# Optimization experiments

Measured on AMD Instinct MI355X. Metric: run time of the kernel, lower is better.

Reference implementation:

```python
import jax, jax.numpy as jnp
import numpy as np

D_MODEL, D_STATE, D_CONV, EXPAND = 1024, 16, 4, 2
D_INNER = EXPAND * D_MODEL
DT_RANK = (D_MODEL + 15) // 16  # 64
B_SZ, SEQ = 2, 1024


def _mamba_dir(x, inW, convW, convB, xpW, dtW, dtB, Alog, Dp, outW):
    """Standard Mamba block forward. x: [B, L, d_model]."""
    Bsz, L, _ = x.shape
    d_inner, d_state = Alog.shape
    dt_rank = xpW.shape[0] - 2 * d_state
    xz = jnp.einsum('bld,ed->ble', x, inW)            # [B, L, 2*d_inner]
    xi, z = jnp.split(xz, 2, axis=-1)
    # depthwise causal conv along L
    xc = jnp.swapaxes(xi, 1, 2)                       # [B, d_inner, L]
    xc = jax.lax.conv_general_dilated(
        xc, convW, window_strides=(1,),
        padding=[(convW.shape[-1] - 1, 0)],
        feature_group_count=d_inner)
    xc = xc + convB[None, :, None]
    u = jax.nn.silu(jnp.swapaxes(xc, 1, 2))           # [B, L, d_inner]
    x_dbl = jnp.einsum('bld,ed->ble', u, xpW)         # [B, L, dt_rank+2N]
    dt, Bm, Cm = jnp.split(x_dbl, [dt_rank, dt_rank + d_state], axis=-1)
    delta = jax.nn.softplus(jnp.einsum('blr,dr->bld', dt, dtW) + dtB)  # [B,L,d_inner]
    A = -jnp.exp(Alog)                                # [d_inner, d_state]

    def step(h, ins):
        d_t, B_t, C_t, u_t = ins                      # [B,D],[B,N],[B,N],[B,D]
        dA = jnp.exp(d_t[:, :, None] * A)             # [B, D, N]
        h = h * dA + (d_t * u_t)[:, :, None] * B_t[:, None, :]
        y_t = jnp.einsum('bdn,bn->bd', h, C_t)
        return h, y_t

    h0 = jnp.zeros((Bsz, d_inner, d_state), x.dtype)
    xs = (jnp.swapaxes(delta, 0, 1), jnp.swapaxes(Bm, 0, 1),
          jnp.swapaxes(Cm, 0, 1), jnp.swapaxes(u, 0, 1))
    _, ys = jax.lax.scan(step, h0, xs)
    y = jnp.swapaxes(ys, 0, 1)                        # [B, L, d_inner]
    y = y + u * Dp
    y = y * jax.nn.silu(z)
    return jnp.einsum('bld,od->blo', y, outW)         # [B, L, d_model]


def _make_params(key, suffix):
    ks = jax.random.split(key, 10)
    s = 0.02
    p = {
        'inW' + suffix: jax.random.normal(ks[0], (2 * D_INNER, D_MODEL), jnp.float32) * s,
        'convW' + suffix: jax.random.normal(ks[1], (D_INNER, 1, D_CONV), jnp.float32) * s,
        'convB' + suffix: jnp.zeros((D_INNER,), jnp.float32),
        'xpW' + suffix: jax.random.normal(ks[2], (DT_RANK + 2 * D_STATE, D_INNER), jnp.float32) * s,
        'dtW' + suffix: jax.random.normal(ks[3], (D_INNER, DT_RANK), jnp.float32) * s,
        'dtB' + suffix: jax.random.normal(ks[4], (D_INNER,), jnp.float32) * 0.1 - 4.0,
        'Alog' + suffix: jnp.log(1.0 + jax.random.uniform(ks[5], (D_INNER, D_STATE), jnp.float32) * 15.0),
        'Dp' + suffix: jnp.ones((D_INNER,), jnp.float32),
        'outW' + suffix: jax.random.normal(ks[6], (D_MODEL, D_INNER), jnp.float32) * s,
    }
    return p


def setup_inputs() -> dict:
    key = jax.random.key(0)
    kx, kf, kb = jax.random.split(key, 3)
    inp = {'x': jax.random.normal(kx, (B_SZ, SEQ, D_MODEL), jnp.float32)}
    inp.update(_make_params(kf, '_f'))
    inp.update(_make_params(kb, '_b'))
    return inp


def reference(x, inW_f, convW_f, convB_f, xpW_f, dtW_f, dtB_f, Alog_f, Dp_f, outW_f,
              inW_b, convW_b, convB_b, xpW_b, dtW_b, dtB_b, Alog_b, Dp_b, outW_b):
    y_fwd = _mamba_dir(x, inW_f, convW_f, convB_f, xpW_f, dtW_f, dtB_f, Alog_f, Dp_f, outW_f)
    xb = jnp.flip(x, axis=1)
    y_bwd = jnp.flip(_mamba_dir(xb, inW_b, convW_b, convB_b, xpW_b, dtW_b, dtB_b, Alog_b, Dp_b, outW_b), axis=1)
    return 0.5 * (y_fwd + y_bwd)
```

## Files before the change

### kernel.cpp

```cpp
#include <hip/hip_runtime.h>
#include <math.h>

#define B_SZ 2
#define SEQ  1024
#define DM   1024
#define DI   2048
#define NST  16
#define RNK  64
#define XPD  96
#define M_TOT (B_SZ*SEQ)
#define NC   32
#define LC   (SEQ/NC)
#define NCH  65536

typedef unsigned short ushort_t;
typedef __attribute__((ext_vector_type(8))) short short8;
typedef __attribute__((ext_vector_type(4))) float f32x4;

#if __has_builtin(__builtin_amdgcn_exp2f)
#define EXP2F __builtin_amdgcn_exp2f
#else
#define EXP2F exp2f
#endif
#define LOG2E 1.44269504f

__device__ __forceinline__ ushort_t f2bf(float f) {
    unsigned u = __float_as_uint(f);
    u += 0x7fff + ((u >> 16) & 1);
    return (ushort_t)(u >> 16);
}
__device__ __forceinline__ float bf2f(ushort_t v) {
    return __uint_as_float(((unsigned)v) << 16);
}

__global__ __launch_bounds__(256)
void convert_all(const float* __restrict__ x,
                 const float* __restrict__ inWf, const float* __restrict__ inWb,
                 const float* __restrict__ outWf, const float* __restrict__ outWb,
                 const float* __restrict__ xpWf, const float* __restrict__ xpWb,
                 ushort_t* __restrict__ xbf, ushort_t* __restrict__ inWcat,
                 ushort_t* __restrict__ outWcat, ushort_t* __restrict__ xpWcat)
{
    int bid = blockIdx.x;
    const float* src; ushort_t* dst; int rel; int strided = 0;
    if (bid < 2048)       { rel = bid;         src = x;     dst = xbf; }
    else if (bid < 6144)  { rel = bid - 2048;  src = inWf;  dst = inWcat; }
    else if (bid < 10240) { rel = bid - 6144;  src = inWb;  dst = inWcat + (size_t)2 * DI * DM; }
    else if (bid < 12288) { rel = bid - 10240; src = outWf; dst = outWcat;      strided = 1; }
    else if (bid < 14336) { rel = bid - 12288; src = outWb; dst = outWcat + DI; strided = 1; }
    else if (bid < 14528) { rel = bid - 14336; src = xpWf;  dst = xpWcat; }
    else                  { rel = bid - 14528; src = xpWb;  dst = xpWcat + (size_t)XPD * DI; }
    int i = rel * 256 + threadIdx.x;
    float4 v = ((const float4*)src)[i];
    ushort4 o;
    o.x = f2bf(v.x); o.y = f2bf(v.y); o.z = f2bf(v.z); o.w = f2bf(v.w);
    if (!strided) {
        ((ushort4*)dst)[i] = o;
    } else {
        int row = i >> 9;
        int c4  = (i - (row << 9)) << 2;
        *(ushort4*)(dst + (size_t)row * (2 * DI) + c4) = o;
    }
}

__device__ __forceinline__ void load_lds16(const ushort_t* g, ushort_t* l) {
    __builtin_amdgcn_global_load_lds(
        (const __attribute__((address_space(1))) void*)g,
        (__attribute__((address_space(3))) void*)l, 16, 0, 0);
}

__device__ __forceinline__ void stageHalf(const ushort_t* g, int grow0, int K, int kt,
                                          ushort_t* lds, int w8, int l8, int gch)
{
    const ushort_t* p = g + (size_t)(grow0 + w8 + l8) * K + (size_t)kt * 64 + (gch << 3);
    load_lds16(p,                  lds + w8 * 64);
    load_lds16(p + (size_t)64 * K, lds + (64 + w8) * 64);
}

__device__ __forceinline__ void rdA4(const ushort_t* buf, int rbase, int sw0, int sw1,
                                     short8 (&a)[4][2])
{
#pragma unroll
    for (int i = 0; i < 4; i++) {
        const ushort_t* p = buf + (size_t)(rbase + i * 16) * 64;
        a[i][0] = *(const short8*)(p + sw0);
        a[i][1] = *(const short8*)(p + sw1);
    }
}
__device__ __forceinline__ void rdB2(const ushort_t* buf, int rbase, int sw0, int sw1,
                                     short8 (&bb)[2][2])
{
#pragma unroll
    for (int j = 0; j < 2; j++) {
        const ushort_t* p = buf + (size_t)(rbase + j * 16) * 64;
        bb[j][0] = *(const short8*)(p + sw0);
        bb[j][1] = *(const short8*)(p + sw1);
    }
}
__device__ __forceinline__ void mm16(const short8 (&a)[4][2], const short8 (&bb)[2][2],
                                     f32x4 (&acc)[4][2])
{
#pragma unroll
    for (int i = 0; i < 4; i++)
#pragma unroll
        for (int j = 0; j < 2; j++) {
            acc[i][j] = __builtin_amdgcn_mfma_f32_16x16x32_bf16(a[i][0], bb[j][0], acc[i][j], 0, 0, 0);
            acc[i][j] = __builtin_amdgcn_mfma_f32_16x16x32_bf16(a[i][1], bb[j][1], acc[i][j], 0, 0, 0);
        }
}

#define BAR()        __builtin_amdgcn_s_barrier()
#define SCHEDB()     __builtin_amdgcn_sched_barrier(0)
#define PRIO1()      __builtin_amdgcn_s_setprio(1)
#define PRIO0()      __builtin_amdgcn_s_setprio(0)
#define WAIT_LGKM0() asm volatile("s_waitcnt lgkmcnt(0)" ::: "memory")
#define WAIT_VM6()   asm volatile("s_waitcnt vmcnt(6)"  ::: "memory")
#define WAIT_VM0()   asm volatile("s_waitcnt vmcnt(0)"  ::: "memory")

__global__ __launch_bounds__(512, 2)
void gemm256_bf16(const ushort_t* __restrict__ A, const ushort_t* __restrict__ W,
                  ushort_t* __restrict__ D, int K, int ldD)
{
    __shared__ __align__(16) ushort_t As[2][256 * 64];
    __shared__ __align__(16) ushort_t Bs[2][256 * 64];

    const int t_   = threadIdx.x;
    const int lane = t_ & 63;
    const int wave = t_ >> 6;
    const int wrq  = wave >> 2;
    const int wcq  = wave & 3;
    const int lm   = lane & 15;
    const int w8   = wave << 3;
    const int l8   = lane >> 3;
    const int gch  = (lane & 7) ^ l8;
    const int sw0  = (((lane >> 4)    ) ^ (lane & 7)) << 3;
    const int sw1  = (((lane >> 4) + 4) ^ (lane & 7)) << 3;

    const int m0 = blockIdx.y * 256;
    const int n0 = blockIdx.x * 256;
    const int NT = K >> 6;

    const int rA0 = wrq * 64 + lm, rA1 = 128 + rA0;
    const int rB0 = wcq * 32 + lm, rB1 = 128 + rB0;

    f32x4 acc[2][2][4][2] = {};
    short8 a[4][2], b0[2][2], b1[2][2];

    stageHalf(A, m0,       K, 0, &As[0][0],        w8, l8, gch);
    stageHalf(A, m0 + 128, K, 0, &As[0][128 * 64], w8, l8, gch);
    stageHalf(W, n0,       K, 0, &Bs[0][0],        w8, l8, gch);
    stageHalf(W, n0 + 128, K, 0, &Bs[0][128 * 64], w8, l8, gch);
    if (NT > 1) {
        stageHalf(A, m0,       K, 1, &As[1][0],        w8, l8, gch);
        stageHalf(W, n0,       K, 1, &Bs[1][0],        w8, l8, gch);
        stageHalf(W, n0 + 128, K, 1, &Bs[1][128 * 64], w8, l8, gch);
        WAIT_VM6();
    } else {
        WAIT_VM0();
    }
    BAR();

    for (int t = 0; t < NT; ++t) {
        const int b = t & 1;
        const ushort_t* Ab = &As[b][0];
        const ushort_t* Bb = &Bs[b][0];
        ushort_t* Abw = &As[b][0];
        ushort_t* Bbw = &Bs[b][0];
        ushort_t* Aow = &As[b ^ 1][0];

        rdA4(Ab, rA0, sw0, sw1, a);
        rdB2(Bb, rB0, sw0, sw1, b0);
        if (t + 1 < NT) stageHalf(A, m0 + 128, K, t + 1, Aow + 128 * 64, w8, l8, gch);
        SCHEDB(); BAR(); WAIT_LGKM0(); SCHEDB();
        PRIO1(); mm16(a, b0, acc[0][0]); PRIO0();
        SCHEDB(); BAR();

        rdB2(Bb, rB1, sw0, sw1, b1);
        if (t + 2 < NT) stageHalf(A, m0, K, t + 2, Abw, w8, l8, gch);
        SCHEDB(); BAR(); WAIT_LGKM0(); SCHEDB();
        PRIO1(); mm16(a, b1, acc[0][1]); PRIO0();
        SCHEDB(); BAR();

        rdA4(Ab, rA1, sw0, sw1, a);
        if (t + 2 < NT) stageHalf(W, n0, K, t + 2, Bbw, w8, l8, gch);
        SCHEDB(); BAR(); WAIT_LGKM0(); SCHEDB();
        PRIO1(); mm16(a, b1, acc[1][1]); PRIO0();
        SCHEDB(); BAR();

        if (t + 2 < NT) stageHalf(W, n0 + 128, K, t + 2, Bbw + 128 * 64, w8, l8, gch);
        SCHEDB(); BAR();
        PRIO1(); mm16(a, b0, acc[1][0]); PRIO0();
        SCHEDB();
        if (t < NT - 2) { WAIT_VM6(); } else { WAIT_VM0(); }
        BAR();
    }

#pragma unroll
    for (int ih = 0; ih < 2; ih++)
#pragma unroll
        for (int i = 0; i < 4; i++)
#pragma unroll
            for (int r = 0; r < 4; r++) {
                int m = m0 + ih * 128 + wrq * 64 + i * 16 + ((lane >> 4) << 2) + r;
#pragma unroll
                for (int jh = 0; jh < 2; jh++)
#pragma unroll
                    for (int j = 0; j < 2; j++) {
                        int n = n0 + jh * 128 + wcq * 32 + j * 16 + lm;
                        D[(size_t)m * ldD + n] = f2bf(acc[ih][jh][i][j][r]);
                    }
            }
}

template<bool OUT_BF16>
__global__ __launch_bounds__(256)
void gemm_gll(const ushort_t* __restrict__ A, const ushort_t* __restrict__ W,
              void* __restrict__ D, int M, int N, int K, int kLen, int ldD)
{
    __shared__ __align__(16) ushort_t As[128 * 64];
    __shared__ __align__(16) ushort_t Ws[128 * 64];
    const int t    = threadIdx.x;
    const int lane = t & 63;
    const int wave = t >> 6;
    const int wr   = (wave >> 1) * 64;
    const int wc   = (wave & 1) * 64;

    const int m0 = blockIdx.y * 128;
    const int n0 = blockIdx.x * 128;
    const int kStart = blockIdx.z * kLen;

    const int srow   = lane >> 3;
    const int gchunk = (lane & 7) ^ srow;

    f32x4 acc[4][4] = {};

    for (int k0 = kStart; k0 < kStart + kLen; k0 += 64) {
#pragma unroll
        for (int it = 0; it < 4; it++) {
            const int rb = wave * 32 + it * 8;
            load_lds16(A + (size_t)(m0 + rb + srow) * K + k0 + gchunk * 8,
                       As + rb * 64);
            load_lds16(W + (size_t)(n0 + rb + srow) * K + k0 + gchunk * 8,
                       Ws + rb * 64);
        }
        __syncthreads();
#pragma unroll
        for (int kk = 0; kk < 2; kk++) {
            const int kc = kk * 4 + (lane >> 4);
            short8 af[4], bf[4];
#pragma unroll
            for (int i = 0; i < 4; i++) {
                int r = wr + i * 16 + (lane & 15);
                af[i] = *(const short8*)(As + r * 64 + ((kc ^ (r & 7)) << 3));
            }
#pragma unroll
            for (int j = 0; j < 4; j++) {
                int r = wc + j * 16 + (lane & 15);
                bf[j] = *(const short8*)(Ws + r * 64 + ((kc ^ (r & 7)) << 3));
            }
#pragma unroll
            for (int i = 0; i < 4; i++)
#pragma unroll
                for (int j = 0; j < 4; j++)
                    acc[i][j] = __builtin_amdgcn_mfma_f32_16x16x32_bf16(
                        af[i], bf[j], acc[i][j], 0, 0, 0);
        }
        __syncthreads();
    }

    if (OUT_BF16) {
        ushort_t* Dp = (ushort_t*)D;
#pragma unroll
        for (int i = 0; i < 4; i++)
#pragma unroll
            for (int r = 0; r < 4; r++) {
                int m = m0 + wr + i * 16 + ((lane >> 4) << 2) + r;
#pragma unroll
                for (int j = 0; j < 4; j++) {
                    int n = n0 + wc + j * 16 + (lane & 15);
                    Dp[(size_t)m * ldD + n] = f2bf(acc[i][j][r]);
                }
            }
    } else {
        float* Dp = (float*)D + (size_t)blockIdx.z * M * ldD;
#pragma unroll
        for (int i = 0; i < 4; i++)
#pragma unroll
            for (int r = 0; r < 4; r++) {
                int m = m0 + wr + i * 16 + ((lane >> 4) << 2) + r;
#pragma unroll
                for (int j = 0; j < 4; j++) {
                    int n = n0 + wc + j * 16 + (lane & 15);
                    Dp[(size_t)m * ldD + n] = acc[i][j][r];
                }
            }
    }
}

__global__ __launch_bounds__(256)
void reduce4(const float* __restrict__ P, float* __restrict__ out)
{
    int i = blockIdx.x * 256 + threadIdx.x;
    const size_t S = (size_t)M_TOT * DM / 4;
    float4 a = ((const float4*)P)[i];
    float4 b = ((const float4*)P)[i + S];
    float4 c = ((const float4*)P)[i + 2 * S];
    float4 d = ((const float4*)P)[i + 3 * S];
    float4 o;
    o.x = 0.5f * (a.x + b.x + c.x + d.x);
    o.y = 0.5f * (a.y + b.y + c.y + d.y);
    o.z = 0.5f * (a.z + b.z + c.z + d.z);
    o.w = 0.5f * (a.w + b.w + c.w + d.w);
    ((float4*)out)[i] = o;
}

#define LDSP 72

__global__ __launch_bounds__(256)
void gemm2_splitk2(const ushort_t* __restrict__ ubf, const ushort_t* __restrict__ xpWcat,
                   float* __restrict__ P)
{
    const int dir = blockIdx.z >> 3;
    const int kz  = blockIdx.z & 7;
    const ushort_t* A = ubf + (size_t)dir * M_TOT * DI;
    const ushort_t* W = xpWcat + (size_t)dir * XPD * DI;
    const int K = DI, N = XPD;

    __shared__ __align__(16) ushort_t As[64 * LDSP];
    __shared__ __align__(16) ushort_t Ws[64 * LDSP];
    const int t    = threadIdx.x;
    const int lane = t & 63;
    const int wave = t >> 6;
    const int wr   = (wave >> 1) * 32;
    const int wc   = (wave & 1) * 32;

    f32x4 acc[2][2] = {};

    const int m0 = blockIdx.y * 64;
    const int n0 = blockIdx.x * 64;
    const int kStart = kz * (DI / 8);
    const int srow = t >> 3;
    const int scol = (t & 7) << 3;

    for (int k0 = kStart; k0 < kStart + DI / 8; k0 += 64) {
        {
            int r = srow;
            short8 v = *(const short8*)(A + (size_t)(m0 + r) * K + k0 + scol);
            *(short8*)(&As[r * LDSP + scol]) = v;
            int r2 = 32 + srow;
            short8 v2 = *(const short8*)(A + (size_t)(m0 + r2) * K + k0 + scol);
            *(short8*)(&As[r2 * LDSP + scol]) = v2;
            int wn = n0 + r;
            short8 wv = {};
            if (wn < N) wv = *(const short8*)(W + (size_t)wn * K + k0 + scol);
            *(short8*)(&Ws[r * LDSP + scol]) = wv;
            int wn2 = n0 + r2;
            short8 wv2 = {};
            if (wn2 < N) wv2 = *(const short8*)(W + (size_t)wn2 * K + k0 + scol);
            *(short8*)(&Ws[r2 * LDSP + scol]) = wv2;
        }
        __syncthreads();
#pragma unroll
        for (int kk = 0; kk < 2; kk++) {
            const int kcol = kk * 32 + ((lane >> 4) << 3);
            short8 af[2], bfr[2];
#pragma unroll
            for (int i = 0; i < 2; i++)
                af[i] = *(const short8*)(&As[(wr + i * 16 + (lane & 15)) * LDSP + kcol]);
#pragma unroll
            for (int j = 0; j < 2; j++)
                bfr[j] = *(const short8*)(&Ws[(wc + j * 16 + (lane & 15)) * LDSP + kcol]);
#pragma unroll
            for (int i = 0; i < 2; i++)
#pragma unroll
                for (int j = 0; j < 2; j++)
                    acc[i][j] = __builtin_amdgcn_mfma_f32_16x16x32_bf16(
                        af[i], bfr[j], acc[i][j], 0, 0, 0);
        }
        __syncthreads();
    }

    float* Pz = P + ((size_t)dir * 8 + kz) * M_TOT * XPD;
#pragma unroll
    for (int i = 0; i < 2; i++)
#pragma unroll
        for (int r = 0; r < 4; r++) {
            int m = m0 + wr + i * 16 + ((lane >> 4) << 2) + r;
#pragma unroll
            for (int j = 0; j < 2; j++) {
                int n = n0 + wc + j * 16 + (lane & 15);
                if (n < N) Pz[(size_t)m * XPD + n] = acc[i][j][r];
            }
        }
}

__global__ __launch_bounds__(256)
void xdbl_reduce2(const float* __restrict__ P, float* __restrict__ xdbl)
{
    int bid = blockIdx.x;
    int dir = bid >= 192;
    int i = (bid - dir * 192) * 256 + threadIdx.x;
    const size_t S = (size_t)M_TOT * XPD / 4;
    const float4* Pd = (const float4*)(P + (size_t)dir * 8 * M_TOT * XPD);
    float4 s = Pd[i];
#pragma unroll
    for (int z = 1; z < 8; z++) {
        float4 v = Pd[i + z * S];
        s.x += v.x; s.y += v.y; s.z += v.z; s.w += v.w;
    }
    ((float4*)(xdbl + (size_t)dir * M_TOT * XPD))[i] = s;
}

__global__ __launch_bounds__(256)
void delta_gemm2(const float* __restrict__ xdbl,
                 const float* __restrict__ dtWf, const float* __restrict__ dtWb,
                 const float* __restrict__ dtBf, const float* __restrict__ dtBb,
                 ushort_t* __restrict__ deltab)
{
    const int dir = blockIdx.z;
    const float* xd  = xdbl + (size_t)dir * M_TOT * XPD;
    const float* dtW = dir ? dtWb : dtWf;
    const float* dtB = dir ? dtBb : dtBf;
    ushort_t* delta  = deltab + (size_t)dir * M_TOT * DI;

    __shared__ __align__(16) ushort_t As[64 * LDSP];
    __shared__ __align__(16) ushort_t Ws[64 * LDSP];
    const int t    = threadIdx.x;
    const int lane = t & 63;
    const int wave = t >> 6;
    const int wr   = (wave >> 1) * 32;
    const int wc   = (wave & 1) * 32;

    const int m0 = blockIdx.y * 64;
    const int n0 = blockIdx.x * 64;
    const int srow = t >> 2;
    const int scol = (t & 3) << 4;

    {
        const float* ap = xd  + (size_t)(m0 + srow) * XPD + scol;
        const float* wp = dtW + (size_t)(n0 + srow) * RNK + scol;
        float4 a[4], w[4];
#pragma unroll
        for (int q = 0; q < 4; q++) { a[q] = ((const float4*)ap)[q]; w[q] = ((const float4*)wp)[q]; }
        __align__(16) ushort_t at[16], wt[16];
#pragma unroll
        for (int q = 0; q < 16; q++) {
            at[q] = f2bf(((const float*)a)[q]);
            wt[q] = f2bf(((const float*)w)[q]);
        }
        *(short8*)(&As[srow * LDSP + scol])     = *(const short8*)(at);
        *(short8*)(&As[srow * LDSP + scol + 8]) = *(const short8*)(at + 8);
        *(short8*)(&Ws[srow * LDSP + scol])     = *(const short8*)(wt);
        *(short8*)(&Ws[srow * LDSP + scol + 8]) = *(const short8*)(wt + 8);
    }
    __syncthreads();

    f32x4 acc[2][2] = {};
#pragma unroll
    for (int kk = 0; kk < 2; kk++) {
        const int kcol = kk * 32 + ((lane >> 4) << 3);
        short8 af[2], bfr[2];
#pragma unroll
        for (int i = 0; i < 2; i++)
            af[i] = *(const short8*)(&As[(wr + i * 16 + (lane & 15)) * LDSP + kcol]);
#pragma unroll
        for (int j = 0; j < 2; j++)
            bfr[j] = *(const short8*)(&Ws[(wc + j * 16 + (lane & 15)) * LDSP + kcol]);
#pragma unroll
        for (int i = 0; i < 2; i++)
#pragma unroll
            for (int j = 0; j < 2; j++)
                acc[i][j] = __builtin_amdgcn_mfma_f32_16x16x32_bf16(
                    af[i], bfr[j], acc[i][j], 0, 0, 0);
    }

#pragma unroll
    for (int j = 0; j < 2; j++) {
        int n = n0 + wc + j * 16 + (lane & 15);
        float bn = dtB[n];
#pragma unroll
        for (int i = 0; i < 2; i++) {
#pragma unroll
            for (int r = 0; r < 4; r++) {
                int m = m0 + wr + i * 16 + ((lane >> 4) << 2) + r;
                float v = acc[i][j][r] + bn;
                float sp = (v > 20.f) ? v : log1pf(__expf(v));
                delta[(size_t)m * DI + n] = f2bf(sp);
            }
        }
    }
}

__global__ __launch_bounds__(256)
void conv_silu2(const ushort_t* __restrict__ xzall,
                const float* __restrict__ convWf, const float* __restrict__ convWb,
                const float* __restrict__ convBf, const float* __restrict__ convBb,
                ushort_t* __restrict__ ubf)
{
    int bid = blockIdx.x;
    int dir = bid >> 12;
    int idx = (bid & 4095) * 256 + threadIdx.x;
    const float* convW = dir ? convWb : convWf;
    const float* convB = dir ? convBb : convBf;
    int di  = (idx & (DI / 4 - 1)) << 2;
    int m   = idx >> 9;
    int b   = m >> 10, l = m & (SEQ - 1);
    const ushort_t* xb = xzall + (size_t)b * SEQ * (4 * DI) + dir * (2 * DI) + di;

    float wv[4][4];
#pragma unroll
    for (int c = 0; c < 4; c++) {
        float4 w = *(const float4*)(convW + (di + c) * 4);
        wv[c][0] = w.x; wv[c][1] = w.y; wv[c][2] = w.z; wv[c][3] = w.w;
    }
    float4 cb = *(const float4*)(convB + di);
    float acc[4] = {cb.x, cb.y, cb.z, cb.w};
#pragma unroll
    for (int j = 0; j < 4; j++) {
        int srcl = dir ? (l + 3 - j) : (l - 3 + j);
        if ((unsigned)srcl < SEQ) {
            ushort4 xv = *(const ushort4*)(xb + (size_t)srcl * (4 * DI));
            acc[0] += wv[0][j] * bf2f(xv.x);
            acc[1] += wv[1][j] * bf2f(xv.y);
            acc[2] += wv[2][j] * bf2f(xv.z);
            acc[3] += wv[3][j] * bf2f(xv.w);
        }
    }
    ushort4 o;
    o.x = f2bf(acc[0] / (1.f + __expf(-acc[0])));
    o.y = f2bf(acc[1] / (1.f + __expf(-acc[1])));
    o.z = f2bf(acc[2] / (1.f + __expf(-acc[2])));
    o.w = f2bf(acc[3] / (1.f + __expf(-acc[3])));
    *(ushort4*)(ubf + (size_t)dir * M_TOT * DI + (size_t)m * DI + di) = o;
}

__global__ __launch_bounds__(256)
void scan_pass1_2(const ushort_t* __restrict__ deltab, const ushort_t* __restrict__ ubf,
                  const float* __restrict__ xdbl,
                  const float* __restrict__ Alogf, const float* __restrict__ Alogb,
                  float* __restrict__ Sb, float* __restrict__ SD)
{
    int tid = threadIdx.x, lane = tid & 63, wv = tid >> 6;
    int blk = blockIdx.x;
    int dir = blk >> 9;
    blk &= 511;
    int dg = blk & 7;
    int bc = blk >> 3;
    int c  = bc & (NC - 1);
    int b  = bc >> 5;
    int d  = (dg * 4 + wv) * 64 + lane;
    int t0 = dir ? (SEQ - 1 - c * LC) : (c * LC);
    int rs = dir ? -1 : 1;

    const float* Alog = dir ? Alogb : Alogf;
    const ushort_t* dl_p = deltab + (size_t)dir * M_TOT * DI;
    const ushort_t* u_p  = ubf    + (size_t)dir * M_TOT * DI;
    const float*    xd   = xdbl   + (size_t)dir * M_TOT * XPD;
    float* Sbd = Sb + (size_t)dir * NC * NCH;
    float* SDd = SD + (size_t)dir * NC * B_SZ * DI;

    float ac2[NST];
#pragma unroll
    for (int q = 0; q < 4; q++) {
        float4 al = *(const float4*)(Alog + (size_t)d * NST + q * 4);
        ac2[q * 4 + 0] = -__expf(al.x) * LOG2E;
        ac2[q * 4 + 1] = -__expf(al.y) * LOG2E;
        ac2[q * 4 + 2] = -__expf(al.z) * LOG2E;
        ac2[q * 4 + 3] = -__expf(al.w) * LOG2E;
    }
    float h[NST];
#pragma unroll
    for (int n = 0; n < NST; n++) h[n] = 0.f;
    float sumD = 0.f;

#pragma unroll 4
    for (int l = 0; l < LC; l++) {
        int t = t0 + rs * l;
        size_t row = (size_t)b * SEQ + t;
        float dl = bf2f(dl_p[row * DI + d]);
        float uv = bf2f(u_p[row * DI + d]);
        const float* xr = xd + row * XPD + RNK;
        float4 Bv[4];
#pragma unroll
        for (int q = 0; q < 4; q++) Bv[q] = *(const float4*)(xr + q * 4);
        float dlu = dl * uv;
        sumD += dl;
#pragma unroll
        for (int n = 0; n < NST; n++) {
            float dA = EXP2F(dl * ac2[n]);
            h[n] = h[n] * dA + dlu * ((const float*)Bv)[n];
        }
    }

    size_t o = (size_t)c * NCH + ((size_t)b * DI + d) * NST;
#pragma unroll
    for (int q = 0; q < 4; q++)
        *(float4*)(Sbd + o + q * 4) = make_float4(h[q*4], h[q*4+1], h[q*4+2], h[q*4+3]);
    SDd[(size_t)c * (B_SZ * DI) + b * DI + d] = sumD;
}

__global__ __launch_bounds__(256)
void scan_combine2(float* __restrict__ Sb, const float* __restrict__ SD,
                   const float* __restrict__ Alogf, const float* __restrict__ Alogb)
{
    int gid = blockIdx.x * 256 + threadIdx.x;
    int dir = gid >= NCH;
    int i = gid - dir * NCH;
    int n = i & 15;
    int d = (i >> 4) & (DI - 1);
    int b = i >> 15;
    const float* Alog = dir ? Alogb : Alogf;
    float* Sbd = Sb + (size_t)dir * NC * NCH;
    const float* SDd = SD + (size_t)dir * NC * B_SZ * DI;
    float ac2 = -__expf(Alog[(size_t)d * NST + n]) * LOG2E;
    float h = 0.f;
#pragma unroll
    for (int c = 0; c < NC; c++) {
        float s = Sbd[(size_t)c * NCH + i];
        float p = EXP2F(ac2 * SDd[(size_t)c * (B_SZ * DI) + b * DI + d]);
        Sbd[(size_t)c * NCH + i] = h;
        h = s + p * h;
    }
}

__global__ __launch_bounds__(256)
void scan_pass2_2(const ushort_t* __restrict__ deltab, const ushort_t* __restrict__ ubf,
                  const float* __restrict__ xdbl, const ushort_t* __restrict__ xzall,
                  const float* __restrict__ Alogf, const float* __restrict__ Alogb,
                  const float* __restrict__ Dpf, const float* __restrict__ Dpb,
                  const float* __restrict__ Hinit, ushort_t* __restrict__ ybf)
{
    int tid = threadIdx.x, lane = tid & 63, wv = tid >> 6;
    int blk = blockIdx.x;
    int dir = blk >> 9;
    blk &= 511;
    int dg = blk & 7;
    int bc = blk >> 3;
    int c  = bc & (NC - 1);
    int b  = bc >> 5;
    int d  = (dg * 4 + wv) * 64 + lane;
    int t0 = dir ? (SEQ - 1 - c * LC) : (c * LC);
    int rs = dir ? -1 : 1;

    const float* Alog = dir ? Alogb : Alogf;
    const float* Dpp  = dir ? Dpb : Dpf;
    const ushort_t* dl_p = deltab + (size_t)dir * M_TOT * DI;
    const ushort_t* u_p  = ubf    + (size_t)dir * M_TOT * DI;
    const float*    xd   = xdbl   + (size_t)dir * M_TOT * XPD;
    const float*    Hin  = Hinit  + (size_t)dir * NC * NCH;

    float ac2[NST];
#pragma unroll
    for (int q = 0; q < 4; q++) {
        float4 al = *(const float4*)(Alog + (size_t)d * NST + q * 4);
        ac2[q * 4 + 0] = -__expf(al.x) * LOG2E;
        ac2[q * 4 + 1] = -__expf(al.y) * LOG2E;
        ac2[q * 4 + 2] = -__expf(al.z) * LOG2E;
        ac2[q * 4 + 3] = -__expf(al.w) * LOG2E;
    }
    float dp = Dpp[d];
    float h[NST];
    {
        size_t o = (size_t)c * NCH + ((size_t)b * DI + d) * NST;
#pragma unroll
        for (int q = 0; q < 4; q++) {
            float4 hv = *(const float4*)(Hin + o + q * 4);
            h[q*4] = hv.x; h[q*4+1] = hv.y; h[q*4+2] = hv.z; h[q*4+3] = hv.w;
        }
    }

#pragma unroll 4
    for (int l = 0; l < LC; l++) {
        int t = t0 + rs * l;
        size_t row = (size_t)b * SEQ + t;
        float dl = bf2f(dl_p[row * DI + d]);
        float uv = bf2f(u_p[row * DI + d]);
        const float* xr = xd + row * XPD + RNK;
        float4 Bv[4], Cv[4];
#pragma unroll
        for (int q = 0; q < 4; q++) {
            Bv[q] = *(const float4*)(xr + q * 4);
            Cv[q] = *(const float4*)(xr + NST + q * 4);
        }
        float dlu = dl * uv;
        float y = 0.f;
#pragma unroll
        for (int n = 0; n < NST; n++) {
            float dA = EXP2F(dl * ac2[n]);
            h[n] = h[n] * dA + dlu * ((const float*)Bv)[n];
            y += h[n] * ((const float*)Cv)[n];
        }
        float z = bf2f(xzall[row * (4 * DI) + dir * (2 * DI) + DI + d]);
        float yv = (y + uv * dp) * (z / (1.f + __expf(-z)));
        ybf[row * (2 * DI) + dir * DI + d] = f2bf(yv);
    }
}

extern "C" void kernel_launch(void* const* d_in, const int* in_sizes, int n_in,
                              void* d_out, int out_size, void* d_ws, size_t ws_size,
                              hipStream_t stream)
{
    char* wsb = (char*)d_ws;

    ushort_t* xzall  = (ushort_t*)wsb;
    ushort_t* ybf    = (ushort_t*)(wsb + 33554432);
    ushort_t* inWcat = (ushort_t*)(wsb + 50331648);
    ushort_t* outWcat= (ushort_t*)(wsb + 67108864);
    ushort_t* xbf    = (ushort_t*)(wsb + 75497472);
    ushort_t* xpWcat = (ushort_t*)(wsb + 79691776);
    ushort_t* ubf    = (ushort_t*)(wsb + 80478208);
    ushort_t* deltab = (ushort_t*)(wsb + 97255424);
    float*    xdbl   = (float*)(wsb + 114032640);

    float* Sb    = (float*)inWcat;
    float* SD    = (float*)xbf;
    float* part2 = (float*)deltab;
    float* part4 = (float*)xzall;

    float* out = (float*)d_out;
    dim3 blk(256);

    convert_all<<<14720, blk, 0, stream>>>(
        (const float*)d_in[0], (const float*)d_in[1], (const float*)d_in[10],
        (const float*)d_in[9], (const float*)d_in[18],
        (const float*)d_in[4], (const float*)d_in[13],
        xbf, inWcat, outWcat, xpWcat);

    gemm256_bf16<<<dim3(8192 / 256, M_TOT / 256), dim3(512), 0, stream>>>(
        xbf, inWcat, xzall, DM, 8192);

    conv_silu2<<<8192, blk, 0, stream>>>(xzall,
        (const float*)d_in[2], (const float*)d_in[11],
        (const float*)d_in[3], (const float*)d_in[12], ubf);

    gemm2_splitk2<<<dim3(2, M_TOT / 64, 16), blk, 0, stream>>>(ubf, xpWcat, part2);

    xdbl_reduce2<<<384, blk, 0, stream>>>(part2, xdbl);

    delta_gemm2<<<dim3(DI / 64, M_TOT / 64, 2), blk, 0, stream>>>(
        xdbl, (const float*)d_in[5], (const float*)d_in[14],
        (const float*)d_in[6], (const float*)d_in[15], deltab);

    scan_pass1_2<<<1024, blk, 0, stream>>>(deltab, ubf, xdbl,
        (const float*)d_in[7], (const float*)d_in[16], Sb, SD);
    scan_combine2<<<2 * NCH / 256, blk, 0, stream>>>(Sb, SD,
        (const float*)d_in[7], (const float*)d_in[16]);
    scan_pass2_2<<<1024, blk, 0, stream>>>(deltab, ubf, xdbl, xzall,
        (const float*)d_in[7], (const float*)d_in[16],
        (const float*)d_in[8], (const float*)d_in[17], Sb, ybf);

    gemm_gll<false><<<dim3(DM / 128, M_TOT / 128, 4), blk, 0, stream>>>(
        ybf, outWcat, part4, M_TOT, DM, 2 * DI, DI / 2, DM);

    reduce4<<<(M_TOT * DM / 4) / 256, blk, 0, stream>>>(part4, out);
}
```

Before: 348.9 us.

## Double scan chunk count and store chunk states in bf16

Raises the number of sequence chunks in the chunked selective scan from 32 to 64, doubling the grid of both scan passes and halving the serial length each thread walks. To keep the extra inter-chunk state traffic down, chunk-end states are stored and combined in bf16 instead of fp32. The combine kernel now runs a longer serial loop over chunks, and bf16 state storage loses precision in the carried hidden state.

Result: faster. 338.8 us (-2.9%).

```diff
diff --git a/kernel.cpp b/kernel.cpp
--- a/kernel.cpp
+++ b/kernel.cpp
@@ -9,7 +9,7 @@
 #define RNK  64
 #define XPD  96
 #define M_TOT (B_SZ*SEQ)
-#define NC   32
+#define NC   64
 #define LC   (SEQ/NC)
 #define NCH  65536
 
@@ -538,16 +538,16 @@
 void scan_pass1_2(const ushort_t* __restrict__ deltab, const ushort_t* __restrict__ ubf,
                   const float* __restrict__ xdbl,
                   const float* __restrict__ Alogf, const float* __restrict__ Alogb,
-                  float* __restrict__ Sb, float* __restrict__ SD)
+                  ushort_t* __restrict__ Sb, float* __restrict__ SD)
 {
     int tid = threadIdx.x, lane = tid & 63, wv = tid >> 6;
     int blk = blockIdx.x;
-    int dir = blk >> 9;
-    blk &= 511;
+    int dir = blk >> 10;
+    blk &= 1023;
     int dg = blk & 7;
     int bc = blk >> 3;
     int c  = bc & (NC - 1);
-    int b  = bc >> 5;
+    int b  = bc >> 6;
     int d  = (dg * 4 + wv) * 64 + lane;
     int t0 = dir ? (SEQ - 1 - c * LC) : (c * LC);
     int rs = dir ? -1 : 1;
@@ -556,7 +556,7 @@
     const ushort_t* dl_p = deltab + (size_t)dir * M_TOT * DI;
     const ushort_t* u_p  = ubf    + (size_t)dir * M_TOT * DI;
     const float*    xd   = xdbl   + (size_t)dir * M_TOT * XPD;
-    float* Sbd = Sb + (size_t)dir * NC * NCH;
+    ushort_t* Sbd = Sb + (size_t)dir * NC * NCH;
     float* SDd = SD + (size_t)dir * NC * B_SZ * DI;
 
     float ac2[NST];
@@ -594,13 +594,19 @@
 
     size_t o = (size_t)c * NCH + ((size_t)b * DI + d) * NST;
 #pragma unroll
-    for (int q = 0; q < 4; q++)
-        *(float4*)(Sbd + o + q * 4) = make_float4(h[q*4], h[q*4+1], h[q*4+2], h[q*4+3]);
+    for (int q = 0; q < 4; q++) {
+        ushort4 pk;
+        pk.x = f2bf(h[q * 4 + 0]);
+        pk.y = f2bf(h[q * 4 + 1]);
+        pk.z = f2bf(h[q * 4 + 2]);
+        pk.w = f2bf(h[q * 4 + 3]);
+        *(ushort4*)(Sbd + o + q * 4) = pk;
+    }
     SDd[(size_t)c * (B_SZ * DI) + b * DI + d] = sumD;
 }
 
 __global__ __launch_bounds__(256)
-void scan_combine2(float* __restrict__ Sb, const float* __restrict__ SD,
+void scan_combine2(ushort_t* __restrict__ Sb, const float* __restrict__ SD,
                    const float* __restrict__ Alogf, const float* __restrict__ Alogb)
 {
     int gid = blockIdx.x * 256 + threadIdx.x;
@@ -610,15 +616,15 @@
     int d = (i >> 4) & (DI - 1);
     int b = i >> 15;
     const float* Alog = dir ? Alogb : Alogf;
-    float* Sbd = Sb + (size_t)dir * NC * NCH;
+    ushort_t* Sbd = Sb + (size_t)dir * NC * NCH;
     const float* SDd = SD + (size_t)dir * NC * B_SZ * DI;
     float ac2 = -__expf(Alog[(size_t)d * NST + n]) * LOG2E;
     float h = 0.f;
 #pragma unroll
     for (int c = 0; c < NC; c++) {
-        float s = Sbd[(size_t)c * NCH + i];
+        float s = bf2f(Sbd[(size_t)c * NCH + i]);
         float p = EXP2F(ac2 * SDd[(size_t)c * (B_SZ * DI) + b * DI + d]);
-        Sbd[(size_t)c * NCH + i] = h;
+        Sbd[(size_t)c * NCH + i] = f2bf(h);
         h = s + p * h;
     }
 }
@@ -628,16 +634,16 @@
                   const float* __restrict__ xdbl, const ushort_t* __restrict__ xzall,
                   const float* __restrict__ Alogf, const float* __restrict__ Alogb,
                   const float* __restrict__ Dpf, const float* __restrict__ Dpb,
-                  const float* __restrict__ Hinit, ushort_t* __restrict__ ybf)
+                  const ushort_t* __restrict__ Hinit, ushort_t* __restrict__ ybf)
 {
     int tid = threadIdx.x, lane = tid & 63, wv = tid >> 6;
     int blk = blockIdx.x;
-    int dir = blk >> 9;
-    blk &= 511;
+    int dir = blk >> 10;
+    blk &= 1023;
     int dg = blk & 7;
     int bc = blk >> 3;
     int c  = bc & (NC - 1);
-    int b  = bc >> 5;
+    int b  = bc >> 6;
     int d  = (dg * 4 + wv) * 64 + lane;
     int t0 = dir ? (SEQ - 1 - c * LC) : (c * LC);
     int rs = dir ? -1 : 1;
@@ -647,7 +653,7 @@
     const ushort_t* dl_p = deltab + (size_t)dir * M_TOT * DI;
     const ushort_t* u_p  = ubf    + (size_t)dir * M_TOT * DI;
     const float*    xd   = xdbl   + (size_t)dir * M_TOT * XPD;
-    const float*    Hin  = Hinit  + (size_t)dir * NC * NCH;
+    const ushort_t* Hin  = Hinit  + (size_t)dir * NC * NCH;
 
     float ac2[NST];
 #pragma unroll
@@ -664,8 +670,11 @@
         size_t o = (size_t)c * NCH + ((size_t)b * DI + d) * NST;
 #pragma unroll
         for (int q = 0; q < 4; q++) {
-            float4 hv = *(const float4*)(Hin + o + q * 4);
-            h[q*4] = hv.x; h[q*4+1] = hv.y; h[q*4+2] = hv.z; h[q*4+3] = hv.w;
+            ushort4 hv = *(const ushort4*)(Hin + o + q * 4);
+            h[q*4]   = bf2f(hv.x);
+            h[q*4+1] = bf2f(hv.y);
+            h[q*4+2] = bf2f(hv.z);
+            h[q*4+3] = bf2f(hv.w);
         }
     }
 
@@ -712,7 +721,7 @@
     ushort_t* deltab = (ushort_t*)(wsb + 97255424);
     float*    xdbl   = (float*)(wsb + 114032640);
 
-    float* Sb    = (float*)inWcat;
+    ushort_t* Sb   = (ushort_t*)inWcat;
     float* SD    = (float*)xbf;
     float* part2 = (float*)deltab;
     float* part4 = (float*)xzall;
@@ -741,11 +750,11 @@
         xdbl, (const float*)d_in[5], (const float*)d_in[14],
         (const float*)d_in[6], (const float*)d_in[15], deltab);
 
-    scan_pass1_2<<<1024, blk, 0, stream>>>(deltab, ubf, xdbl,
+    scan_pass1_2<<<2048, blk, 0, stream>>>(deltab, ubf, xdbl,
         (const float*)d_in[7], (const float*)d_in[16], Sb, SD);
     scan_combine2<<<2 * NCH / 256, blk, 0, stream>>>(Sb, SD,
         (const float*)d_in[7], (const float*)d_in[16]);
-    scan_pass2_2<<<1024, blk, 0, stream>>>(deltab, ubf, xdbl, xzall,
+    scan_pass2_2<<<2048, blk, 0, stream>>>(deltab, ubf, xdbl, xzall,
         (const float*)d_in[7], (const float*)d_in[16],
         (const float*)d_in[8], (const float*)d_in[17], Sb, ybf);
 
```
